# Kernel optimization log

Measured on AMD Instinct MI355X. Metric: run time of the kernel, lower is better.

## Reference

```python
import jax, jax.numpy as jnp
import numpy as np

N = 20000      # total nodes
E = 160000     # total edges
G = 64         # graphs in batch
D_ESM = 1280
D = 512
OUT = 500
NUM_LAYERS = 3


def setup_inputs() -> dict:
    key = jax.random.key(0)
    ks = jax.random.split(key, 16)
    s = 0.02
    inp = {
        "native_x": jax.random.randint(ks[0], (N,), 0, 21),
        "x": jax.random.normal(ks[1], (N, D_ESM), dtype=jnp.float32),
        "edge_index": jax.random.randint(ks[2], (2, E), 0, N),
        "batch": jnp.sort(jax.random.randint(ks[3], (N,), 0, G)),
        # parameters
        "embed_table": jax.random.normal(ks[4], (21, 96), dtype=jnp.float32) * s,
        "proj_aa_w": jax.random.normal(ks[5], (96, D), dtype=jnp.float32) * s,
        "proj_aa_b": jnp.zeros((D,), jnp.float32),
        "proj_esm_w": jax.random.normal(ks[6], (D_ESM, D), dtype=jnp.float32) * s,
        "proj_esm_b": jnp.zeros((D,), jnp.float32),
        "gcn_w": jax.random.normal(ks[7], (NUM_LAYERS, D, D), dtype=jnp.float32) * s,
        "gcn_b": jnp.zeros((NUM_LAYERS, D), jnp.float32),
        "ro1_w": jax.random.normal(ks[8], (D, 1024), dtype=jnp.float32) * s,
        "ro1_b": jnp.zeros((1024,), jnp.float32),
        "ro2_w": jax.random.normal(ks[9], (1024, OUT), dtype=jnp.float32) * s,
        "ro2_b": jnp.zeros((OUT,), jnp.float32),
        "weight1": jnp.array([0.6, 0.4], jnp.float32),
    }
    return inp


def _gcn_stack(feat, src, dst, enorm, self_norm, gcn_w, gcn_b):
    # GraphCNN: 3 GCNConv layers (PyG: sym-normalized adj with self loops),
    # residual add after the first layer.
    for i in range(NUM_LAYERS):
        hW = feat @ gcn_w[i]                                   # [N, D]
        msg = hW[src] * enorm[:, None]                          # [E, D] gather
        agg = jax.ops.segment_sum(msg, dst, num_segments=N)     # scatter-add
        agg = agg + hW * self_norm[:, None] + gcn_b[i]
        out = jax.nn.relu(agg)
        feat = out if i == 0 else feat + out
    return feat


def reference(native_x, x, edge_index, batch, embed_table,
              proj_aa_w, proj_aa_b, proj_esm_w, proj_esm_b,
              gcn_w, gcn_b, ro1_w, ro1_b, ro2_w, ro2_b, weight1):
    # embedding + projections (dropout = identity, eval mode)
    x_aa = embed_table[native_x] @ proj_aa_w + proj_aa_b        # [N, 512]
    x_esm_lin = x @ proj_esm_w + proj_esm_b                     # [N, 512]
    h = jax.nn.relu(x_aa + x_esm_lin)
    x_esm = jax.nn.relu(x_esm_lin)

    src, dst = edge_index[0], edge_index[1]
    # GCN normalization with self loops: deg over targets + 1
    deg = jax.ops.segment_sum(jnp.ones((E,), x.dtype), dst, num_segments=N) + 1.0
    dis = deg ** -0.5
    enorm = dis[src] * dis[dst]     # per-edge norm
    self_norm = dis * dis           # self-loop norm

    n1 = _gcn_stack(h, src, dst, enorm, self_norm, gcn_w, gcn_b)
    n3 = _gcn_stack(x_esm, src, dst, enorm, self_norm, gcn_w, gcn_b)

    # global max pool per graph
    g1 = jax.ops.segment_max(n1, batch, num_segments=G)          # [G, 512]
    g3 = jax.ops.segment_max(n3, batch, num_segments=G)

    g = weight1[0] * g1 + weight1[1] * g3
    y = jax.nn.sigmoid(jax.nn.relu(g @ ro1_w + ro1_b) @ ro2_w + ro2_b)
    return y
```

## Files before the change

### kernel.cpp

```cpp
#include <hip/hip_runtime.h>
#include <float.h>

#define NN 20000
#define EE 160000
#define GG 64
#define DD 512
#define NL 3
#define M2 40000
#define M2P 40064
#define M1 20000
#define M1P 20096
#define BK 64

typedef __bf16 bf16x8 __attribute__((ext_vector_type(8)));
typedef float f32x4 __attribute__((ext_vector_type(4)));
typedef unsigned int u32;
typedef unsigned short u16;
typedef u32 u32x4 __attribute__((ext_vector_type(4)));
typedef u32 u32x2 __attribute__((ext_vector_type(2)));

union FragU { u32x4 u; bf16x8 b; };

__device__ inline float blo(u32 u){ union{u32 i;float f;}x; x.i=u<<16; return x.f; }
__device__ inline float bhi(u32 u){ union{u32 i;float f;}x; x.i=u&0xFFFF0000u; return x.f; }
__device__ inline float bf2f(u16 v){ union{u32 i;float f;}x; x.i=((u32)v)<<16; return x.f; }
__device__ inline u16 f2bf(float f){ union{float f;u32 i;}x; x.f=f; u32 r=x.i+0x7FFFu+((x.i>>16)&1u); return (u16)(r>>16); }
__device__ inline u32 pack2(float a,float b){ return (u32)f2bf(a) | ((u32)f2bf(b)<<16); }

__device__ __forceinline__ void gload16(const void* g, void* lds){
  __builtin_amdgcn_global_load_lds(
    (const __attribute__((address_space(1))) void*)g,
    (__attribute__((address_space(3))) void*)lds, 16, 0, 0);
}

__device__ __forceinline__ void acc8(float* a, uint4 q, float w){
  a[0]+=w*blo(q.x); a[1]+=w*bhi(q.x);
  a[2]+=w*blo(q.y); a[3]+=w*bhi(q.y);
  a[4]+=w*blo(q.z); a[5]+=w*bhi(q.z);
  a[6]+=w*blo(q.w); a[7]+=w*bhi(q.w);
}

__global__ void k_cvt(const float* __restrict__ in, u16* __restrict__ outp){
  int t = blockIdx.x*256+threadIdx.x;
  if(t >= M1P*160) return;
  int row = t/160, gidx = t%160;
  u32x4 o;
  if(row < M1){
    const float* s = in + (size_t)row*1280 + gidx*8;
    float4 v0 = *(const float4*)s;
    float4 v1 = *(const float4*)(s+4);
    o.x=pack2(v0.x,v0.y); o.y=pack2(v0.z,v0.w);
    o.z=pack2(v1.x,v1.y); o.w=pack2(v1.z,v1.w);
  } else {
    o.x=o.y=o.z=o.w=0u;
  }
  *(u32x4*)(outp + (size_t)row*1280 + gidx*8) = o;
}

__global__ void k_transpose_cvt(const float* __restrict__ in, u16* __restrict__ outp, int R, int C){
  __shared__ float t[32][33];
  int c0 = blockIdx.x*32, r0 = blockIdx.y*32;
  t[threadIdx.y][threadIdx.x] = in[(size_t)(r0+threadIdx.y)*C + c0+threadIdx.x];
  __syncthreads();
  outp[(size_t)(c0+threadIdx.y)*R + r0+threadIdx.x] = f2bf(t[threadIdx.x][threadIdx.y]);
}

__global__ void k_transpose_f32(const float* __restrict__ in, float* __restrict__ outp, int R, int C){
  __shared__ float t[32][33];
  int c0 = blockIdx.x*32, r0 = blockIdx.y*32;
  int r = r0+threadIdx.y, c = c0+threadIdx.x;
  if(r<R && c<C) t[threadIdx.y][threadIdx.x] = in[(size_t)r*C + c];
  __syncthreads();
  int oc = c0+threadIdx.y, orr = r0+threadIdx.x;
  if(oc<C && orr<R) outp[(size_t)oc*R + orr] = t[threadIdx.x][threadIdx.y];
}

__global__ void k_embp(const float* __restrict__ et, const float* __restrict__ w,
                       const float* __restrict__ b, float* __restrict__ outp){
  int t = blockIdx.x*256+threadIdx.x;
  if(t >= 21*512) return;
  int a = t>>9, d = t&511;
  float s = b[d];
  for(int k=0;k<96;k++) s += et[a*96+k]*w[k*512+d];
  outp[t] = s;
}

__global__ void k_deg(const int* __restrict__ ei, int* __restrict__ deg){
  int e = blockIdx.x*256+threadIdx.x; if(e>=EE) return;
  atomicAdd(&deg[ei[EE+e]], 1);
}
__global__ void k_dis(const int* __restrict__ deg, float* __restrict__ dis){
  int n = blockIdx.x*256+threadIdx.x; if(n>=NN) return;
  dis[n] = rsqrtf((float)deg[n] + 1.0f);
}
__global__ void k_scan(const int* __restrict__ deg, int* __restrict__ offs){
  __shared__ int part[1024];
  int tid = threadIdx.x;
  int base = tid*20;
  int s=0;
  for(int i=0;i<20;i++){ int idx=base+i; if(idx<NN) s += deg[idx]; }
  part[tid]=s; __syncthreads();
  for(int off=1; off<1024; off<<=1){
    int v = (tid>=off)? part[tid-off] : 0;
    __syncthreads();
    part[tid] += v;
    __syncthreads();
  }
  int pre = (tid>0)? part[tid-1] : 0;
  for(int i=0;i<20;i++){ int idx=base+i; if(idx<NN){ offs[idx]=pre; pre += deg[idx]; } }
  if(tid==1023) offs[NN]=part[1023];
}
__global__ void k_fill(const int* __restrict__ ei, const int* __restrict__ offs, int* __restrict__ curs,
                       const float* __restrict__ dis, int* __restrict__ csrs, float* __restrict__ csrw){
  int e = blockIdx.x*256+threadIdx.x; if(e>=EE) return;
  int s = ei[e], d = ei[EE+e];
  int pos = atomicAdd(&curs[d],1);
  int slot = offs[d]+pos;
  csrs[slot]=s;
  csrw[slot]=dis[s]*dis[d];
}

__global__ __launch_bounds__(256) void k_gemm(const u16* __restrict__ A, const u16* __restrict__ Bt,
                                              u16* __restrict__ C, int Mstore, int K, int lda){
  __shared__ u16 lsA[128*BK];
  __shared__ u16 lsB[128*BK];
  const int tid = threadIdx.x;
  const int lane = tid & 63;
  const int wid = tid >> 6;
  const int wr = wid >> 1, wc = wid & 1;
  const int la = lane & 15, lg = lane >> 4;
  const int n0 = blockIdx.x * 128;
  const int rowB = blockIdx.y * 128;

  f32x4 acc[4][4];
  #pragma unroll
  for(int m=0;m<4;m++)
    #pragma unroll
    for(int n=0;n<4;n++)
      #pragma unroll
      for(int r=0;r<4;r++) acc[m][n][r]=0.f;

  const u16* Arow = A + (size_t)rowB*lda;
  const u16* Brow = Bt + (size_t)n0*K;

  int srow[4], scol[4], ldsoff[4];
  #pragma unroll
  for(int i=0;i<4;i++){
    int li = i*256+tid;
    srow[i] = li>>3;
    scol[i] = ((li&7) ^ (srow[i]&7))*8;
    ldsoff[i] = (i*256 + wid*64)*8;
  }

  for(int k0=0;k0<K;k0+=BK){
    #pragma unroll
    for(int i=0;i<4;i++)
      gload16(Arow + (size_t)srow[i]*lda + k0 + scol[i], lsA + ldsoff[i]);
    #pragma unroll
    for(int i=0;i<4;i++)
      gload16(Brow + (size_t)srow[i]*K + k0 + scol[i], lsB + ldsoff[i]);
    __syncthreads();
    #pragma unroll
    for(int kk=0;kk<2;kk++){
      FragU aF[4], bF[4];
      #pragma unroll
      for(int m=0;m<4;m++){
        int row = wr*64+m*16+la;
        aF[m].u = *(const u32x4*)&lsA[row*BK + ((kk*4+lg)^(row&7))*8];
      }
      #pragma unroll
      for(int n=0;n<4;n++){
        int row = wc*64+n*16+la;
        bF[n].u = *(const u32x4*)&lsB[row*BK + ((kk*4+lg)^(row&7))*8];
      }
      #pragma unroll
      for(int m=0;m<4;m++)
        #pragma unroll
        for(int n=0;n<4;n++)
          acc[m][n] = __builtin_amdgcn_mfma_f32_16x16x32_bf16(aF[m].b, bF[n].b, acc[m][n], 0,0,0);
    }
    __syncthreads();
  }
  #pragma unroll
  for(int m=0;m<4;m++)
    #pragma unroll
    for(int n=0;n<4;n++)
      #pragma unroll
      for(int r=0;r<4;r++){
        int rr = rowB + wr*64 + m*16 + lg*4 + r;
        if(rr < Mstore)
          C[(size_t)rr*512 + n0 + wc*64 + n*16 + la] = f2bf(acc[m][n][r]);
      }
}

__global__ void k_fuse(const u16* __restrict__ xW, const int* __restrict__ nx,
                       const float* __restrict__ embp, const float* __restrict__ esm_b,
                       u16* __restrict__ feat){
  int t = blockIdx.x*256+threadIdx.x;
  if(t >= NN*64) return;
  int n = t>>6, c = (t&63)*8;
  uint4 q = *(const uint4*)(xW + (size_t)n*512 + c);
  int a = nx[n];
  float xw[8] = {blo(q.x),bhi(q.x),blo(q.y),bhi(q.y),blo(q.z),bhi(q.z),blo(q.w),bhi(q.w)};
  float h[8], ee[8];
  #pragma unroll
  for(int j=0;j<8;j++){
    float t1 = xw[j] + esm_b[c+j];
    float hh = embp[a*512 + c + j] + t1;
    h[j]  = hh>0.f?hh:0.f;
    ee[j] = t1>0.f?t1:0.f;
  }
  uint4 o1, o2;
  o1.x=pack2(h[0],h[1]); o1.y=pack2(h[2],h[3]); o1.z=pack2(h[4],h[5]); o1.w=pack2(h[6],h[7]);
  o2.x=pack2(ee[0],ee[1]); o2.y=pack2(ee[2],ee[3]); o2.z=pack2(ee[4],ee[5]); o2.w=pack2(ee[6],ee[7]);
  *(uint4*)(feat + (size_t)(2*n)*512 + c) = o1;
  *(uint4*)(feat + (size_t)(2*n+1)*512 + c) = o2;
}

__global__ __launch_bounds__(64) void k_agg2(const u16* __restrict__ hW, u16* __restrict__ feat,
                 const int* __restrict__ offs, const int* __restrict__ csrs,
                 const float* __restrict__ csrw, const float* __restrict__ dis,
                 const float* __restrict__ bias, int layer){
  const int nn = blockIdx.x;
  const int lane = threadIdx.x;
  const size_t co = (size_t)lane*8;
  const int e0 = offs[nn], e1 = offs[nn+1];
  float a1[8]={0,0,0,0,0,0,0,0}, a3[8]={0,0,0,0,0,0,0,0};

  const u16* ps = hW + (size_t)(2*nn)*512 + co;
  uint4 qs1 = *(const uint4*)ps;
  uint4 qs3 = *(const uint4*)(ps + 512);
  float dn = dis[nn], sn = dn*dn;

  int e = e0;
  for(; e+1 < e1; e += 2){
    int sA = csrs[e],   sB = csrs[e+1];
    float wA = csrw[e], wB = csrw[e+1];
    const u16* pA = hW + (size_t)(2*sA)*512 + co;
    const u16* pB = hW + (size_t)(2*sB)*512 + co;
    uint4 qA1 = *(const uint4*)pA;
    uint4 qA3 = *(const uint4*)(pA + 512);
    uint4 qB1 = *(const uint4*)pB;
    uint4 qB3 = *(const uint4*)(pB + 512);
    acc8(a1,qA1,wA); acc8(a3,qA3,wA);
    acc8(a1,qB1,wB); acc8(a3,qB3,wB);
  }
  if(e < e1){
    int sA = csrs[e]; float wA = csrw[e];
    const u16* pA = hW + (size_t)(2*sA)*512 + co;
    uint4 qA1 = *(const uint4*)pA;
    uint4 qA3 = *(const uint4*)(pA + 512);
    acc8(a1,qA1,wA); acc8(a3,qA3,wA);
  }
  acc8(a1,qs1,sn); acc8(a3,qs3,sn);

  float4 b0 = *(const float4*)(bias + lane*8);
  float4 b1 = *(const float4*)(bias + lane*8 + 4);
  a1[0]+=b0.x; a1[1]+=b0.y; a1[2]+=b0.z; a1[3]+=b0.w;
  a1[4]+=b1.x; a1[5]+=b1.y; a1[6]+=b1.z; a1[7]+=b1.w;
  a3[0]+=b0.x; a3[1]+=b0.y; a3[2]+=b0.z; a3[3]+=b0.w;
  a3[4]+=b1.x; a3[5]+=b1.y; a3[6]+=b1.z; a3[7]+=b1.w;
  #pragma unroll
  for(int j=0;j<8;j++){ a1[j] = a1[j]>0.f?a1[j]:0.f; a3[j] = a3[j]>0.f?a3[j]:0.f; }
  if(layer>0){
    const u16* pf = feat + (size_t)(2*nn)*512 + co;
    uint4 qf1 = *(const uint4*)pf;
    uint4 qf3 = *(const uint4*)(pf + 512);
    acc8(a1,qf1,1.f); acc8(a3,qf3,1.f);
  }
  uint4 o1, o3;
  o1.x=pack2(a1[0],a1[1]); o1.y=pack2(a1[2],a1[3]); o1.z=pack2(a1[4],a1[5]); o1.w=pack2(a1[6],a1[7]);
  o3.x=pack2(a3[0],a3[1]); o3.y=pack2(a3[2],a3[3]); o3.z=pack2(a3[4],a3[5]); o3.w=pack2(a3[6],a3[7]);
  u16* po = feat + (size_t)(2*nn)*512 + co;
  *(uint4*)po = o1;
  *(uint4*)(po + 512) = o3;
}

__global__ void k_bounds(const int* __restrict__ batch, int* __restrict__ starts){
  int n = blockIdx.x*256+threadIdx.x;
  if(n>=NN) return;
  int b = batch[n];
  int pb = n ? batch[n-1] : -1;
  for(int g=pb+1; g<=b; g++) starts[g]=n;
  if(n==NN-1){ for(int g=b+1; g<=GG; g++) starts[g]=NN; }
}

__global__ void k_pool(const u16* __restrict__ feat, const int* __restrict__ starts,
                       u32* __restrict__ m1, u32* __restrict__ m3){
  int g = blockIdx.x, c = blockIdx.y;
  int s = starts[g], e = starts[g+1];
  int len = e - s;
  int b0 = s + (len*c)/8, b1 = s + (len*(c+1))/8;
  int t = threadIdx.x;
  float a0=0.f, a1=0.f, c0=0.f, c1=0.f;
  for(int n=b0;n<b1;++n){
    const u16* pr = feat + (size_t)(2*n)*512 + t*2;
    u32 q1 = *(const u32*)pr;
    u32 q3 = *(const u32*)(pr + 512);
    a0 = fmaxf(a0, blo(q1)); a1 = fmaxf(a1, bhi(q1));
    c0 = fmaxf(c0, blo(q3)); c1 = fmaxf(c1, bhi(q3));
  }
  atomicMax(m1 + g*512 + t*2,     __float_as_uint(a0));
  atomicMax(m1 + g*512 + t*2 + 1, __float_as_uint(a1));
  atomicMax(m3 + g*512 + t*2,     __float_as_uint(c0));
  atomicMax(m3 + g*512 + t*2 + 1, __float_as_uint(c1));
}
__global__ void k_gcomb(const u32* __restrict__ m1, const u32* __restrict__ m3,
                        const float* __restrict__ w1, float* __restrict__ gc){
  int t = blockIdx.x*256+threadIdx.x; if(t>=GG*512) return;
  gc[t] = w1[0]*__uint_as_float(m1[t]) + w1[1]*__uint_as_float(m3[t]);
}

__global__ __launch_bounds__(256) void k_ro1v(const float* __restrict__ gc, const float* __restrict__ wT,
                                              const float* __restrict__ b, float* __restrict__ r1){
  int gw = blockIdx.x*4 + (threadIdx.x>>6);
  int g = gw >> 10, o = gw & 1023;
  int lane = threadIdx.x & 63;
  const float4* gr = (const float4*)(gc + (size_t)g*512);
  const float4* wr = (const float4*)(wT + (size_t)o*512);
  float s = 0.f;
  #pragma unroll
  for(int i=0;i<2;i++){
    float4 a = gr[i*64+lane];
    float4 w = wr[i*64+lane];
    s += a.x*w.x + a.y*w.y + a.z*w.z + a.w*w.w;
  }
  #pragma unroll
  for(int m=32;m>=1;m>>=1) s += __shfl_xor(s, m, 64);
  if(lane==0){ s += b[o]; r1[gw] = s>0.f ? s : 0.f; }
}
__global__ __launch_bounds__(256) void k_ro2v(const float* __restrict__ r1, const float* __restrict__ wT,
                                              const float* __restrict__ b, float* __restrict__ y){
  int gw = blockIdx.x*4 + (threadIdx.x>>6);
  int g = gw/500, o = gw - g*500;
  int lane = threadIdx.x & 63;
  const float4* gr = (const float4*)(r1 + (size_t)g*1024);
  const float4* wr = (const float4*)(wT + (size_t)o*1024);
  float s = 0.f;
  #pragma unroll
  for(int i=0;i<4;i++){
    float4 a = gr[i*64+lane];
    float4 w = wr[i*64+lane];
    s += a.x*w.x + a.y*w.y + a.z*w.z + a.w*w.w;
  }
  #pragma unroll
  for(int m=32;m>=1;m>>=1) s += __shfl_xor(s, m, 64);
  if(lane==0) y[gw] = 1.0f/(1.0f+__expf(-(s + b[o])));
}

extern "C" void kernel_launch(void* const* d_in, const int* in_sizes, int n_in,
                              void* d_out, int out_size, void* d_ws, size_t ws_size,
                              hipStream_t stream){
  const int*   native_x = (const int*)d_in[0];
  const float* x        = (const float*)d_in[1];
  const int*   ei       = (const int*)d_in[2];
  const int*   batch    = (const int*)d_in[3];
  const float* embed_t  = (const float*)d_in[4];
  const float* paa_w    = (const float*)d_in[5];
  const float* paa_b    = (const float*)d_in[6];
  const float* pesm_w   = (const float*)d_in[7];
  const float* pesm_b   = (const float*)d_in[8];
  const float* gcn_w    = (const float*)d_in[9];
  const float* gcn_b    = (const float*)d_in[10];
  const float* ro1_w    = (const float*)d_in[11];
  const float* ro1_b    = (const float*)d_in[12];
  const float* ro2_w    = (const float*)d_in[13];
  const float* ro2_b    = (const float*)d_in[14];
  const float* w1       = (const float*)d_in[15];
  float* out = (float*)d_out;

  char* p = (char*)d_ws;
  auto alloc = [&](size_t n){ void* r = (void*)p; p += (n + 255) & ~(size_t)255; return r; };
  u16* feat   = (u16*)alloc((size_t)M2P*512*2);
  u16* hW     = (u16*)alloc((size_t)M2P*512*2);
  u16* xbf    = (u16*)alloc((size_t)M1P*1280*2);
  u16* WtE    = (u16*)alloc((size_t)512*1280*2);
  u16* WtG    = (u16*)alloc((size_t)3*512*512*2);
  float* roT1 = (float*)alloc((size_t)1024*512*4);
  float* roT2 = (float*)alloc((size_t)500*1024*4);
  float* embp = (float*)alloc(21*512*4);
  int* deg    = (int*)alloc(NN*4);
  float* dis  = (float*)alloc(NN*4);
  int* offs   = (int*)alloc((NN+1)*4);
  int* curs   = (int*)alloc(NN*4);
  int* csrs   = (int*)alloc(EE*4);
  float* csrw = (float*)alloc(EE*4);
  int* starts = (int*)alloc((GG+1)*4);
  u32* m1b    = (u32*)alloc(GG*512*4);
  u32* m3b    = (u32*)alloc(GG*512*4);
  float* gc   = (float*)alloc(GG*512*4);
  float* r1   = (float*)alloc(GG*1024*4);
  (void)ws_size; (void)in_sizes; (void)n_in; (void)out_size;

  hipMemsetAsync(deg,  0, NN*4, stream);
  hipMemsetAsync(curs, 0, NN*4, stream);
  hipMemsetAsync(m1b,  0, GG*512*4, stream);
  hipMemsetAsync(m3b,  0, GG*512*4, stream);

  k_cvt<<<(M1P*160+255)/256,256,0,stream>>>(x, xbf);
  k_transpose_cvt<<<dim3(16,40),dim3(32,32),0,stream>>>(pesm_w, WtE, 1280, 512);
  for(int i=0;i<3;i++)
    k_transpose_cvt<<<dim3(16,16),dim3(32,32),0,stream>>>(gcn_w+(size_t)i*262144, WtG+(size_t)i*262144, 512, 512);
  k_transpose_f32<<<dim3(32,16),dim3(32,32),0,stream>>>(ro1_w, roT1, 512, 1024);
  k_transpose_f32<<<dim3(16,32),dim3(32,32),0,stream>>>(ro2_w, roT2, 1024, 500);
  k_embp<<<42,256,0,stream>>>(embed_t, paa_w, paa_b, embp);
  k_deg<<<(EE+255)/256,256,0,stream>>>(ei, deg);
  k_dis<<<(NN+255)/256,256,0,stream>>>(deg, dis);
  k_scan<<<1,1024,0,stream>>>(deg, offs);
  k_fill<<<(EE+255)/256,256,0,stream>>>(ei, offs, curs, dis, csrs, csrw);

  k_gemm<<<dim3(4,157),256,0,stream>>>(xbf, WtE, hW, M1, 1280, 1280);
  k_fuse<<<(NN*64+255)/256,256,0,stream>>>(hW, native_x, embp, pesm_b, feat);

  for(int i=0;i<3;i++){
    k_gemm<<<dim3(4,313),256,0,stream>>>(feat, WtG+(size_t)i*262144, hW, M2, 512, 512);
    k_agg2<<<NN,64,0,stream>>>(hW, feat, offs, csrs, csrw, dis, gcn_b+(size_t)i*512, i);
  }

  k_bounds<<<(NN+255)/256,256,0,stream>>>(batch, starts);
  k_pool<<<dim3(GG,8),256,0,stream>>>(feat, starts, m1b, m3b);
  k_gcomb<<<(GG*512+255)/256,256,0,stream>>>(m1b, m3b, w1, gc);
  k_ro1v<<<16384,256,0,stream>>>(gc, roT1, ro1_b, r1);
  k_ro2v<<<8000,256,0,stream>>>(r1, roT2, ro2_b, out);
}
```

Baseline: 494.6 us.

## Fuse epilogues, pooling and readout combine; pack CSR edge data

Folds the projection/ReLU epilogue into the first GEMM, fuses the degree-normalisation into the scan, merges the three weight transposes into one launch, and fuses global max pooling into the last aggregation via atomicMax, dropping bounds/pool/gcomb kernels. Edge source offsets and weights are packed into one int2 array to halve index loads in the gather. This cuts launches and a full feature pass, but the fused pooling issues many atomics per node.

```diff
diff --git a/kernel.cpp b/kernel.cpp
--- a/kernel.cpp
+++ b/kernel.cpp
@@ -23,7 +23,6 @@
 
 __device__ inline float blo(u32 u){ union{u32 i;float f;}x; x.i=u<<16; return x.f; }
 __device__ inline float bhi(u32 u){ union{u32 i;float f;}x; x.i=u&0xFFFF0000u; return x.f; }
-__device__ inline float bf2f(u16 v){ union{u32 i;float f;}x; x.i=((u32)v)<<16; return x.f; }
 __device__ inline u16 f2bf(float f){ union{float f;u32 i;}x; x.f=f; u32 r=x.i+0x7FFFu+((x.i>>16)&1u); return (u16)(r>>16); }
 __device__ inline u32 pack2(float a,float b){ return (u32)f2bf(a) | ((u32)f2bf(b)<<16); }
 
@@ -57,8 +56,11 @@
   *(u32x4*)(outp + (size_t)row*1280 + gidx*8) = o;
 }
 
-__global__ void k_transpose_cvt(const float* __restrict__ in, u16* __restrict__ outp, int R, int C){
+__global__ void k_transpose_cvt(const float* __restrict__ in, u16* __restrict__ outp, int R, int C,
+                                size_t zin, size_t zout){
   __shared__ float t[32][33];
+  in   += (size_t)blockIdx.z * zin;
+  outp += (size_t)blockIdx.z * zout;
   int c0 = blockIdx.x*32, r0 = blockIdx.y*32;
   t[threadIdx.y][threadIdx.x] = in[(size_t)(r0+threadIdx.y)*C + c0+threadIdx.x];
   __syncthreads();
@@ -89,16 +91,15 @@
   int e = blockIdx.x*256+threadIdx.x; if(e>=EE) return;
   atomicAdd(&deg[ei[EE+e]], 1);
 }
-__global__ void k_dis(const int* __restrict__ deg, float* __restrict__ dis){
-  int n = blockIdx.x*256+threadIdx.x; if(n>=NN) return;
-  dis[n] = rsqrtf((float)deg[n] + 1.0f);
-}
-__global__ void k_scan(const int* __restrict__ deg, int* __restrict__ offs){
+__global__ void k_scan(const int* __restrict__ deg, int* __restrict__ offs, float* __restrict__ dis){
   __shared__ int part[1024];
   int tid = threadIdx.x;
   int base = tid*20;
   int s=0;
-  for(int i=0;i<20;i++){ int idx=base+i; if(idx<NN) s += deg[idx]; }
+  for(int i=0;i<20;i++){
+    int idx=base+i;
+    if(idx<NN){ int dv = deg[idx]; s += dv; dis[idx] = rsqrtf((float)dv + 1.0f); }
+  }
   part[tid]=s; __syncthreads();
   for(int off=1; off<1024; off<<=1){
     int v = (tid>=off)? part[tid-off] : 0;
@@ -111,17 +112,18 @@
   if(tid==1023) offs[NN]=part[1023];
 }
 __global__ void k_fill(const int* __restrict__ ei, const int* __restrict__ offs, int* __restrict__ curs,
-                       const float* __restrict__ dis, int* __restrict__ csrs, float* __restrict__ csrw){
+                       const float* __restrict__ dis, int2* __restrict__ edat){
   int e = blockIdx.x*256+threadIdx.x; if(e>=EE) return;
   int s = ei[e], d = ei[EE+e];
   int pos = atomicAdd(&curs[d],1);
-  int slot = offs[d]+pos;
-  csrs[slot]=s;
-  csrw[slot]=dis[s]*dis[d];
-}
-
+  edat[offs[d]+pos] = make_int2(s*2048, __float_as_int(dis[s]*dis[d]));
+}
+
+template<int EPI>
 __global__ __launch_bounds__(256) void k_gemm(const u16* __restrict__ A, const u16* __restrict__ Bt,
-                                              u16* __restrict__ C, int Mstore, int K, int lda){
+                                              u16* __restrict__ C, int Mstore, int K, int lda,
+                                              const int* __restrict__ nx, const float* __restrict__ embp,
+                                              const float* __restrict__ esm_b){
   __shared__ u16 lsA[128*BK];
   __shared__ u16 lsB[128*BK];
   const int tid = threadIdx.x;
@@ -184,72 +186,63 @@
   #pragma unroll
   for(int m=0;m<4;m++)
     #pragma unroll
-    for(int n=0;n<4;n++)
-      #pragma unroll
-      for(int r=0;r<4;r++){
-        int rr = rowB + wr*64 + m*16 + lg*4 + r;
-        if(rr < Mstore)
-          C[(size_t)rr*512 + n0 + wc*64 + n*16 + la] = f2bf(acc[m][n][r]);
+    for(int r=0;r<4;r++){
+      int rr = rowB + wr*64 + m*16 + lg*4 + r;
+      if(rr < Mstore){
+        int aidx = (EPI==1) ? nx[rr] : 0;
+        #pragma unroll
+        for(int n=0;n<4;n++){
+          int col = n0 + wc*64 + n*16 + la;
+          float v = acc[m][n][r];
+          if(EPI==0){
+            C[(size_t)rr*512 + col] = f2bf(v);
+          } else {
+            float t1 = v + esm_b[col];
+            float hh = embp[aidx*512 + col] + t1;
+            C[(size_t)(2*rr)*512 + col]   = f2bf(hh>0.f?hh:0.f);
+            C[(size_t)(2*rr+1)*512 + col] = f2bf(t1>0.f?t1:0.f);
+          }
+        }
       }
-}
-
-__global__ void k_fuse(const u16* __restrict__ xW, const int* __restrict__ nx,
-                       const float* __restrict__ embp, const float* __restrict__ esm_b,
-                       u16* __restrict__ feat){
-  int t = blockIdx.x*256+threadIdx.x;
-  if(t >= NN*64) return;
-  int n = t>>6, c = (t&63)*8;
-  uint4 q = *(const uint4*)(xW + (size_t)n*512 + c);
-  int a = nx[n];
-  float xw[8] = {blo(q.x),bhi(q.x),blo(q.y),bhi(q.y),blo(q.z),bhi(q.z),blo(q.w),bhi(q.w)};
-  float h[8], ee[8];
-  #pragma unroll
-  for(int j=0;j<8;j++){
-    float t1 = xw[j] + esm_b[c+j];
-    float hh = embp[a*512 + c + j] + t1;
-    h[j]  = hh>0.f?hh:0.f;
-    ee[j] = t1>0.f?t1:0.f;
-  }
-  uint4 o1, o2;
-  o1.x=pack2(h[0],h[1]); o1.y=pack2(h[2],h[3]); o1.z=pack2(h[4],h[5]); o1.w=pack2(h[6],h[7]);
-  o2.x=pack2(ee[0],ee[1]); o2.y=pack2(ee[2],ee[3]); o2.z=pack2(ee[4],ee[5]); o2.w=pack2(ee[6],ee[7]);
-  *(uint4*)(feat + (size_t)(2*n)*512 + c) = o1;
-  *(uint4*)(feat + (size_t)(2*n+1)*512 + c) = o2;
-}
-
+    }
+}
+
+template<int MODE>
 __global__ __launch_bounds__(64) void k_agg2(const u16* __restrict__ hW, u16* __restrict__ feat,
-                 const int* __restrict__ offs, const int* __restrict__ csrs,
-                 const float* __restrict__ csrw, const float* __restrict__ dis,
-                 const float* __restrict__ bias, int layer){
+                 const int* __restrict__ offs, const int2* __restrict__ edat,
+                 const float* __restrict__ dis, const float* __restrict__ bias,
+                 const int* __restrict__ batch, u32* __restrict__ m1b, u32* __restrict__ m3b){
   const int nn = blockIdx.x;
   const int lane = threadIdx.x;
-  const size_t co = (size_t)lane*8;
+  const int co = lane*16;
+  const char* base = (const char*)hW;
   const int e0 = offs[nn], e1 = offs[nn+1];
   float a1[8]={0,0,0,0,0,0,0,0}, a3[8]={0,0,0,0,0,0,0,0};
 
-  const u16* ps = hW + (size_t)(2*nn)*512 + co;
+  const char* ps = base + (size_t)nn*2048 + co;
   uint4 qs1 = *(const uint4*)ps;
-  uint4 qs3 = *(const uint4*)(ps + 512);
+  uint4 qs3 = *(const uint4*)(ps + 1024);
   float dn = dis[nn], sn = dn*dn;
 
   int e = e0;
   for(; e+1 < e1; e += 2){
-    int sA = csrs[e],   sB = csrs[e+1];
-    float wA = csrw[e], wB = csrw[e+1];
-    const u16* pA = hW + (size_t)(2*sA)*512 + co;
-    const u16* pB = hW + (size_t)(2*sB)*512 + co;
+    int2 edA = edat[e], edB = edat[e+1];
+    const char* pA = base + (u32)edA.x + co;
+    const char* pB = base + (u32)edB.x + co;
     uint4 qA1 = *(const uint4*)pA;
-    uint4 qA3 = *(const uint4*)(pA + 512);
+    uint4 qA3 = *(const uint4*)(pA + 1024);
     uint4 qB1 = *(const uint4*)pB;
-    uint4 qB3 = *(const uint4*)(pB + 512);
+    uint4 qB3 = *(const uint4*)(pB + 1024);
+    float wA = __int_as_float(edA.y), wB = __int_as_float(edB.y);
     acc8(a1,qA1,wA); acc8(a3,qA3,wA);
     acc8(a1,qB1,wB); acc8(a3,qB3,wB);
   }
   if(e < e1){
-    int sA = csrs[e]; float wA = csrw[e];
-    const u16* pA = hW + (size_t)(2*sA)*512 + co;
+    int2 edA = edat[e];
+    const char* pA = base + (u32)edA.x + co;
     uint4 qA1 = *(const uint4*)pA;
-    uint4 qA3 = *(const uint4*)(pA + 512);
+    uint4 qA3 = *(const uint4*)(pA + 1024);
+    float wA = __int_as_float(edA.y);
     acc8(a1,qA1,wA); acc8(a3,qA3,wA);
   }
   acc8(a1,qs1,sn); acc8(a3,qs3,sn);
@@ -262,68 +255,50 @@
   a3[4]+=b1.x; a3[5]+=b1.y; a3[6]+=b1.z; a3[7]+=b1.w;
   #pragma unroll
   for(int j=0;j<8;j++){ a1[j] = a1[j]>0.f?a1[j]:0.f; a3[j] = a3[j]>0.f?a3[j]:0.f; }
-  if(layer>0){
-    const u16* pf = feat + (size_t)(2*nn)*512 + co;
+  if(MODE>0){
+    const char* pf = (const char*)feat + (size_t)nn*2048 + co;
     uint4 qf1 = *(const uint4*)pf;
-    uint4 qf3 = *(const uint4*)(pf + 512);
+    uint4 qf3 = *(const uint4*)(pf + 1024);
     acc8(a1,qf1,1.f); acc8(a3,qf3,1.f);
   }
-  uint4 o1, o3;
-  o1.x=pack2(a1[0],a1[1]); o1.y=pack2(a1[2],a1[3]); o1.z=pack2(a1[4],a1[5]); o1.w=pack2(a1[6],a1[7]);
-  o3.x=pack2(a3[0],a3[1]); o3.y=pack2(a3[2],a3[3]); o3.z=pack2(a3[4],a3[5]); o3.w=pack2(a3[6],a3[7]);
-  u16* po = feat + (size_t)(2*nn)*512 + co;
-  *(uint4*)po = o1;
-  *(uint4*)(po + 512) = o3;
-}
-
-__global__ void k_bounds(const int* __restrict__ batch, int* __restrict__ starts){
-  int n = blockIdx.x*256+threadIdx.x;
-  if(n>=NN) return;
-  int b = batch[n];
-  int pb = n ? batch[n-1] : -1;
-  for(int g=pb+1; g<=b; g++) starts[g]=n;
-  if(n==NN-1){ for(int g=b+1; g<=GG; g++) starts[g]=NN; }
-}
-
-__global__ void k_pool(const u16* __restrict__ feat, const int* __restrict__ starts,
-                       u32* __restrict__ m1, u32* __restrict__ m3){
-  int g = blockIdx.x, c = blockIdx.y;
-  int s = starts[g], e = starts[g+1];
-  int len = e - s;
-  int b0 = s + (len*c)/8, b1 = s + (len*(c+1))/8;
-  int t = threadIdx.x;
-  float a0=0.f, a1=0.f, c0=0.f, c1=0.f;
-  for(int n=b0;n<b1;++n){
-    const u16* pr = feat + (size_t)(2*n)*512 + t*2;
-    u32 q1 = *(const u32*)pr;
-    u32 q3 = *(const u32*)(pr + 512);
-    a0 = fmaxf(a0, blo(q1)); a1 = fmaxf(a1, bhi(q1));
-    c0 = fmaxf(c0, blo(q3)); c1 = fmaxf(c1, bhi(q3));
-  }
-  atomicMax(m1 + g*512 + t*2,     __float_as_uint(a0));
-  atomicMax(m1 + g*512 + t*2 + 1, __float_as_uint(a1));
-  atomicMax(m3 + g*512 + t*2,     __float_as_uint(c0));
-  atomicMax(m3 + g*512 + t*2 + 1, __float_as_uint(c1));
-}
-__global__ void k_gcomb(const u32* __restrict__ m1, const u32* __restrict__ m3,
-                        const float* __restrict__ w1, float* __restrict__ gc){
-  int t = blockIdx.x*256+threadIdx.x; if(t>=GG*512) return;
-  gc[t] = w1[0]*__uint_as_float(m1[t]) + w1[1]*__uint_as_float(m3[t]);
-}
-
-__global__ __launch_bounds__(256) void k_ro1v(const float* __restrict__ gc, const float* __restrict__ wT,
+  if(MODE<2){
+    uint4 o1, o3;
+    o1.x=pack2(a1[0],a1[1]); o1.y=pack2(a1[2],a1[3]); o1.z=pack2(a1[4],a1[5]); o1.w=pack2(a1[6],a1[7]);
+    o3.x=pack2(a3[0],a3[1]); o3.y=pack2(a3[2],a3[3]); o3.z=pack2(a3[4],a3[5]); o3.w=pack2(a3[6],a3[7]);
+    char* po = (char*)feat + (size_t)nn*2048 + co;
+    *(uint4*)po = o1;
+    *(uint4*)(po + 1024) = o3;
+  } else {
+    int g = batch[nn];
+    u32* p1 = m1b + g*512 + lane*8;
+    u32* p3 = m3b + g*512 + lane*8;
+    #pragma unroll
+    for(int j=0;j<8;j++) atomicMax(p1+j, __float_as_uint(a1[j]));
+    #pragma unroll
+    for(int j=0;j<8;j++) atomicMax(p3+j, __float_as_uint(a3[j]));
+  }
+}
+
+__global__ __launch_bounds__(256) void k_ro1v(const u32* __restrict__ m1b, const u32* __restrict__ m3b,
+                                              const float* __restrict__ w1, const float* __restrict__ wT,
                                               const float* __restrict__ b, float* __restrict__ r1){
   int gw = blockIdx.x*4 + (threadIdx.x>>6);
   int g = gw >> 10, o = gw & 1023;
   int lane = threadIdx.x & 63;
-  const float4* gr = (const float4*)(gc + (size_t)g*512);
+  float w10 = w1[0], w11 = w1[1];
+  const uint4* g1 = (const uint4*)(m1b + (size_t)g*512);
+  const uint4* g3 = (const uint4*)(m3b + (size_t)g*512);
   const float4* wr = (const float4*)(wT + (size_t)o*512);
   float s = 0.f;
   #pragma unroll
   for(int i=0;i<2;i++){
-    float4 a = gr[i*64+lane];
+    uint4 q1 = g1[i*64+lane];
+    uint4 q3 = g3[i*64+lane];
     float4 w = wr[i*64+lane];
-    s += a.x*w.x + a.y*w.y + a.z*w.z + a.w*w.w;
+    s += (w10*__uint_as_float(q1.x) + w11*__uint_as_float(q3.x))*w.x;
+    s += (w10*__uint_as_float(q1.y) + w11*__uint_as_float(q3.y))*w.y;
+    s += (w10*__uint_as_float(q1.z) + w11*__uint_as_float(q3.z))*w.z;
+    s += (w10*__uint_as_float(q1.w) + w11*__uint_as_float(q3.w))*w.w;
   }
   #pragma unroll
   for(int m=32;m>=1;m>>=1) s += __shfl_xor(s, m, 64);
@@ -383,43 +358,35 @@
   float* dis  = (float*)alloc(NN*4);
   int* offs   = (int*)alloc((NN+1)*4);
   int* curs   = (int*)alloc(NN*4);
-  int* csrs   = (int*)alloc(EE*4);
-  float* csrw = (float*)alloc(EE*4);
-  int* starts = (int*)alloc((GG+1)*4);
+  int2* edat  = (int2*)alloc((size_t)EE*8);
   u32* m1b    = (u32*)alloc(GG*512*4);
   u32* m3b    = (u32*)alloc(GG*512*4);
-  float* gc   = (float*)alloc(GG*512*4);
   float* r1   = (float*)alloc(GG*1024*4);
   (void)ws_size; (void)in_sizes; (void)n_in; (void)out_size;
 
   hipMemsetAsync(deg,  0, NN*4, stream);
   hipMemsetAsync(curs, 0, NN*4, stream);
-  hipMemsetAsync(m1b,  0, GG*512*4, stream);
-  hipMemsetAsync(m3b,  0, GG*512*4, stream);
+  hipMemsetAsync(m1b,  0, 2*GG*512*4, stream);
 
   k_cvt<<<(M1P*160+255)/256,256,0,stream>>>(x, xbf);
-  k_transpose_cvt<<<dim3(16,40),dim3(32,32),0,stream>>>(pesm_w, WtE, 1280, 512);
-  for(int i=0;i<3;i++)
-    k_transpose_cvt<<<dim3(16,16),dim3(32,32),0,stream>>>(gcn_w+(size_t)i*262144, WtG+(size_t)i*262144, 512, 512);
+  k_transpose_cvt<<<dim3(16,40,1),dim3(32,32),0,stream>>>(pesm_w, WtE, 1280, 512, 0, 0);
+  k_transpose_cvt<<<dim3(16,16,3),dim3(32,32),0,stream>>>(gcn_w, WtG, 512, 512, 262144, 262144);
   k_transpose_f32<<<dim3(32,16),dim3(32,32),0,stream>>>(ro1_w, roT1, 512, 1024);
   k_transpose_f32<<<dim3(16,32),dim3(32,32),0,stream>>>(ro2_w, roT2, 1024, 500);
   k_embp<<<42,256,0,stream>>>(embed_t, paa_w, paa_b, embp);
   k_deg<<<(EE+255)/256,256,0,stream>>>(ei, deg);
-  k_dis<<<(NN+255)/256,256,0,stream>>>(deg, dis);
-  k_scan<<<1,1024,0,stream>>>(deg, offs);
-  k_fill<<<(EE+255)/256,256,0,stream>>>(ei, offs, curs, dis, csrs, csrw);
-
-  k_gemm<<<dim3(4,157),256,0,stream>>>(xbf, WtE, hW, M1, 1280, 1280);
-  k_fuse<<<(NN*64+255)/256,256,0,stream>>>(hW, native_x, embp, pesm_b, feat);
-
-  for(int i=0;i<3;i++){
-    k_gemm<<<dim3(4,313),256,0,stream>>>(feat, WtG+(size_t)i*262144, hW, M2, 512, 512);
-    k_agg2<<<NN,64,0,stream>>>(hW, feat, offs, csrs, csrw, dis, gcn_b+(size_t)i*512, i);
-  }
-
-  k_bounds<<<(NN+255)/256,256,0,stream>>>(batch, starts);
-  k_pool<<<dim3(GG,8),256,0,stream>>>(feat, starts, m1b, m3b);
-  k_gcomb<<<(GG*512+255)/256,256,0,stream>>>(m1b, m3b, w1, gc);
-  k_ro1v<<<16384,256,0,stream>>>(gc, roT1, ro1_b, r1);
+  k_scan<<<1,1024,0,stream>>>(deg, offs, dis);
+  k_fill<<<(EE+255)/256,256,0,stream>>>(ei, offs, curs, dis, edat);
+
+  k_gemm<1><<<dim3(4,157),256,0,stream>>>(xbf, WtE, feat, M1, 1280, 1280, native_x, embp, pesm_b);
+
+  k_gemm<0><<<dim3(4,313),256,0,stream>>>(feat, WtG,            hW, M2, 512, 512, nullptr, nullptr, nullptr);
+  k_agg2<0><<<NN,64,0,stream>>>(hW, feat, offs, edat, dis, gcn_b,       batch, m1b, m3b);
+  k_gemm<0><<<dim3(4,313),256,0,stream>>>(feat, WtG+262144,     hW, M2, 512, 512, nullptr, nullptr, nullptr);
+  k_agg2<1><<<NN,64,0,stream>>>(hW, feat, offs, edat, dis, gcn_b+512,   batch, m1b, m3b);
+  k_gemm<0><<<dim3(4,313),256,0,stream>>>(feat, WtG+2*262144,   hW, M2, 512, 512, nullptr, nullptr, nullptr);
+  k_agg2<2><<<NN,64,0,stream>>>(hW, feat, offs, edat, dis, gcn_b+1024,  batch, m1b, m3b);
+
+  k_ro1v<<<16384,256,0,stream>>>(m1b, m3b, w1, roT1, ro1_b, r1);
   k_ro2v<<<8000,256,0,stream>>>(r1, roT2, ro2_b, out);
 }
```

New measurement: 967.3 us. 1.96x slower.
